# Kernel optimization log

Hardware: AMD Instinct MI355X
Metric: run time of the kernel (lower is better)

## Reference

```python
import jax, jax.numpy as jnp
import numpy as np

B, N, C = 8, 1024, 1024
H = 16
D = C // H  # head_dim = 64
SCALE = D ** -0.5


def setup_inputs() -> dict:
    key = jax.random.key(0)
    k1, k2, k3, k4 = jax.random.split(key, 4)
    x = jax.random.normal(k1, (B, N, C), dtype=jnp.float32)
    qkv_w = jax.random.normal(k2, (3 * C, C), dtype=jnp.float32) * (C ** -0.5)
    proj_w = jax.random.normal(k3, (C, C), dtype=jnp.float32) * (C ** -0.5)
    proj_b = jax.random.normal(k4, (C,), dtype=jnp.float32)
    return {"x": x, "qkv_w": qkv_w, "proj_w": proj_w, "proj_b": proj_b}


def reference(x, qkv_w, proj_w, proj_b):
    # qkv projection: torch Linear weight is [out, in] -> x @ W^T
    qkv = jnp.einsum('bnc,oc->bno', x, qkv_w)            # [B, N, 3C]
    qkv = qkv.reshape(B, N, 3, H, D)
    q = jnp.transpose(qkv[:, :, 0], (0, 2, 1, 3))        # [B, H, N, D]
    k = jnp.transpose(qkv[:, :, 1], (0, 2, 1, 3))
    v = jnp.transpose(qkv[:, :, 2], (0, 2, 1, 3))
    attn = jnp.einsum('bhqd,bhkd->bhqk', q, k) * SCALE   # [B, H, N, N]
    attn = jax.nn.softmax(attn, axis=-1)
    out = jnp.einsum('bhqk,bhkd->bhqd', attn, v)         # [B, H, N, D]
    out = jnp.transpose(out, (0, 2, 1, 3)).reshape(B, N, C)
    out = jnp.einsum('bnc,oc->bno', out, proj_w) + proj_b
    return out
```

## Files before the change

### kernel.cpp

```cpp
#include <hip/hip_runtime.h>
#include <hip/hip_bf16.h>
#include <stdint.h>

#define B_ 8
#define N_ 1024
#define C_ 1024
#define H_ 16

static constexpr float SCALE = 0.125f;
static constexpr float LOG2E = 1.4426950408889634f;
static constexpr float SL    = SCALE * LOG2E;

typedef __attribute__((ext_vector_type(4))) float f32x4;
typedef __attribute__((ext_vector_type(8))) short s16x8;

__device__ __forceinline__ ushort f2bf(float f) {
    union { float f; uint32_t u; } c; c.f = f;
    uint32_t u = c.u;
    return (ushort)((u + 0x7fffu + ((u >> 16) & 1u)) >> 16);
}

__device__ __forceinline__ ushort f2bfc(float f) {
    union { __hip_bfloat16 h; ushort u; } c;
    c.h = __float2bfloat16(f);
    return c.u;
}

__device__ __forceinline__ void gload_lds16(const void* g, void* l) {
    __builtin_amdgcn_global_load_lds(
        (const __attribute__((address_space(1))) void*)g,
        (__attribute__((address_space(3))) void*)l,
        16, 0, 0);
}
__device__ __forceinline__ void gload_lds4(const void* g, void* l) {
    __builtin_amdgcn_global_load_lds(
        (const __attribute__((address_space(1))) void*)g,
        (__attribute__((address_space(3))) void*)l,
        4, 0, 0);
}

__global__ __launch_bounds__(256) void cvt_all(const float* __restrict__ x,
                                               const float* __restrict__ qkv_w,
                                               const float* __restrict__ proj_w,
                                               ushort* __restrict__ xb,
                                               ushort* __restrict__ wqkv,
                                               ushort* __restrict__ wproj) {
    int i = blockIdx.x * 256 + threadIdx.x;
    const float* src;
    ushort* dst;
    float sc = 1.0f;
    if (i < 2097152) {
        src = x; dst = xb;
    } else if (i < 2097152 + 786432) {
        i -= 2097152;
        src = qkv_w; dst = wqkv;
        if (i < 262144) sc = SL;
    } else {
        i -= 2097152 + 786432;
        src = proj_w; dst = wproj;
    }
    float4 v = ((const float4*)src)[i];
    ushort4 o = make_ushort4(f2bf(v.x * sc), f2bf(v.y * sc), f2bf(v.z * sc), f2bf(v.w * sc));
    ((ushort4*)dst)[i] = o;
}

template<int OUT_BF16>
__global__ __launch_bounds__(256) void gemm_bt(const ushort* __restrict__ A,
                                               const ushort* __restrict__ Bw,
                                               void* __restrict__ Cout,
                                               const float* __restrict__ bias,
                                               int M, int Nout, int K) {
    __shared__ ushort Asm[128 * 64];
    __shared__ ushort Bsm[128 * 64];
    const int t = threadIdx.x;
    const int l = t & 63, w = t >> 6;
    const int lq = l & 15, lg = l >> 4;
    const int trow = blockIdx.y * 128, tcol = blockIdx.x * 128;
    const int wrow = (w >> 1) * 64, wcol = (w & 1) * 64;

    f32x4 acc[4][4] = {};

    const int srow0 = t >> 3;
    const int sc8 = (((t & 7) ^ (srow0 & 7)) * 8);
    const size_t abase = (size_t)(trow + srow0) * K + sc8;
    const size_t bbase = (size_t)(tcol + srow0) * K + sc8;

    for (int k0 = 0; k0 < K; k0 += 64) {
#pragma unroll
        for (int i = 0; i < 4; ++i) {
            gload_lds16(A + abase + (size_t)i * 32 * K + k0, &Asm[(i * 256 + w * 64) * 8]);
            gload_lds16(Bw + bbase + (size_t)i * 32 * K + k0, &Bsm[(i * 256 + w * 64) * 8]);
        }
        __syncthreads();
#pragma unroll
        for (int kk = 0; kk < 2; ++kk) {
            s16x8 af[4], bf[4];
#pragma unroll
            for (int m = 0; m < 4; ++m) {
                int row = wrow + m * 16 + lq;
                int ch = (kk * 4 + lg) ^ (row & 7);
                af[m] = *(const s16x8*)&Asm[row * 64 + ch * 8];
            }
#pragma unroll
            for (int n = 0; n < 4; ++n) {
                int row = wcol + n * 16 + lq;
                int ch = (kk * 4 + lg) ^ (row & 7);
                bf[n] = *(const s16x8*)&Bsm[row * 64 + ch * 8];
            }
#pragma unroll
            for (int m = 0; m < 4; ++m)
#pragma unroll
                for (int n = 0; n < 4; ++n)
                    acc[m][n] = __builtin_amdgcn_mfma_f32_16x16x32_bf16(af[m], bf[n], acc[m][n], 0, 0, 0);
        }
        __syncthreads();
    }

#pragma unroll
    for (int m = 0; m < 4; ++m)
#pragma unroll
        for (int n = 0; n < 4; ++n)
#pragma unroll
            for (int r = 0; r < 4; ++r) {
                int row = trow + wrow + m * 16 + lg * 4 + r;
                int col = tcol + wcol + n * 16 + lq;
                if (OUT_BF16) {
                    ((ushort*)Cout)[(size_t)row * Nout + col] = f2bfc(acc[m][n][r]);
                } else {
                    ((float*)Cout)[(size_t)row * Nout + col] = acc[m][n][r] + bias[col];
                }
            }
}

__global__ __launch_bounds__(512, 2) void gemm_bt256(const ushort* __restrict__ A,
                                                     const ushort* __restrict__ Bw,
                                                     ushort* __restrict__ Cout,
                                                     int M, int Nout, int K) {
    __shared__ ushort Asm[2][256 * 64];
    __shared__ ushort Bsm[2][256 * 64];
    const int t = threadIdx.x;
    const int l = t & 63, w = t >> 6;
    const int lq = l & 15, lg = l >> 4;
    const int wm = w >> 2, wn = w & 3;

    int bid = blockIdx.y * gridDim.x + blockIdx.x;
    const int cpx = (gridDim.x * gridDim.y) >> 3;
    bid = (bid & 7) * cpx + (bid >> 3);
    const int bx = bid % gridDim.x, by = bid / gridDim.x;
    const int trow = by * 256, tcol = bx * 256;

    f32x4 acc[8][4] = {};

    const int srow = t >> 3;
    const int scc = ((t & 7) ^ (srow & 7)) * 8;
    const size_t abase = (size_t)(trow + srow) * K + scc;
    const size_t bbase = (size_t)(tcol + srow) * K + scc;

#define STAGE256(buf, k0)                                                      \
    {                                                                          \
        _Pragma("unroll")                                                      \
        for (int j = 0; j < 4; ++j) {                                          \
            gload_lds16(A + abase + (size_t)j * 64 * K + (k0),                 \
                        &Asm[buf][(j * 512 + t) * 8]);                         \
            gload_lds16(Bw + bbase + (size_t)j * 64 * K + (k0),                \
                        &Bsm[buf][(j * 512 + t) * 8]);                         \
        }                                                                      \
    }
#define LOAD_A256(qr)                                                          \
    _Pragma("unroll") for (int m = 0; m < 4; ++m) {                            \
        const int row = wm * 128 + (qr) * 64 + m * 16 + lq;                    \
        _Pragma("unroll") for (int kk = 0; kk < 2; ++kk)                       \
            af[m][kk] = *(const s16x8*)&Asm[cur][row * 64 +                    \
                            (((kk * 4 + lg) ^ (row & 7)) * 8)];                \
    }
#define LOAD_B256(qc)                                                          \
    _Pragma("unroll") for (int n = 0; n < 2; ++n) {                            \
        const int row = wn * 64 + (qc) * 32 + n * 16 + lq;                     \
        _Pragma("unroll") for (int kk = 0; kk < 2; ++kk)                       \
            bf[n][kk] = *(const s16x8*)&Bsm[cur][row * 64 +                    \
                            (((kk * 4 + lg) ^ (row & 7)) * 8)];                \
    }
#define MFMA_Q256(qr, qc)                                                      \
    __builtin_amdgcn_s_setprio(1);                                             \
    _Pragma("unroll") for (int m = 0; m < 4; ++m)                              \
        _Pragma("unroll") for (int n = 0; n < 2; ++n)                          \
            _Pragma("unroll") for (int kk = 0; kk < 2; ++kk)                   \
                acc[(qr) * 4 + m][(qc) * 2 + n] =                              \
                    __builtin_amdgcn_mfma_f32_16x16x32_bf16(                   \
                        af[m][kk], bf[n][kk], acc[(qr) * 4 + m][(qc) * 2 + n], \
                        0, 0, 0);                                              \
    __builtin_amdgcn_s_setprio(0);

    STAGE256(0, 0);
    asm volatile("s_waitcnt vmcnt(0)" ::: "memory");
    __builtin_amdgcn_s_barrier();

    const int NT = K / 64;
    for (int kt = 0; kt < NT; ++kt) {
        const int cur = kt & 1, nxt = cur ^ 1;
        s16x8 af[4][2], bf[2][2];
        LOAD_A256(0); LOAD_B256(0);
        if (kt < NT - 1) STAGE256(nxt, (kt + 1) * 64);
        __builtin_amdgcn_s_barrier();
        MFMA_Q256(0, 0);
        __builtin_amdgcn_s_barrier();
        LOAD_B256(1);
        __builtin_amdgcn_s_barrier();
        MFMA_Q256(0, 1);
        __builtin_amdgcn_s_barrier();
        LOAD_A256(1);
        __builtin_amdgcn_s_barrier();
        MFMA_Q256(1, 1);
        __builtin_amdgcn_s_barrier();
        LOAD_B256(0);
        __builtin_amdgcn_s_barrier();
        MFMA_Q256(1, 0);
        asm volatile("s_waitcnt vmcnt(0)" ::: "memory");
        __builtin_amdgcn_s_barrier();
    }

#pragma unroll
    for (int mt = 0; mt < 8; ++mt)
#pragma unroll
        for (int nt = 0; nt < 4; ++nt)
#pragma unroll
            for (int r = 0; r < 4; ++r) {
                int row = trow + wm * 128 + mt * 16 + lg * 4 + r;
                int col = tcol + wn * 64 + nt * 16 + lq;
                Cout[(size_t)row * Nout + col] = f2bfc(acc[mt][nt][r]);
            }
#undef STAGE256
#undef LOAD_A256
#undef LOAD_B256
#undef MFMA_Q256
}

__global__ __launch_bounds__(512) void attn_fwd(const ushort* __restrict__ qk,
                                                const ushort* __restrict__ vt,
                                                ushort* __restrict__ attn_out) {
    __shared__ ushort Klds[64 * 64];
    __shared__ ushort Vlds[64 * 64];

    const int t = threadIdx.x, l = t & 63, w = t >> 6;
    const int lq = l & 15, lg = l >> 4;

    const int serial = blockIdx.x + 8 * blockIdx.y;
    const int logical = (serial & 7) * 128 + (serial >> 3);
    const int qt = logical & 7;
    const int bh = logical >> 3;
    const int b = bh >> 4, h = bh & 15;

    const int qrow = qt * 128 + w * 16 + lq;
    const size_t qoff = (size_t)(b * N_ + qrow) * 2048 + h * 64;
    const s16x8 qf0 = *(const s16x8*)&qk[qoff + lg * 8];
    const s16x8 qf1 = *(const s16x8*)&qk[qoff + 32 + lg * 8];

    float l_run = 0.f;
    f32x4 o[4] = {};

    const int srow0 = t >> 3;
    const int sc8 = ((t & 7) ^ (srow0 & 7)) * 8;
    const size_t kgbase = (size_t)(b * N_ + srow0) * 2048 + 1024 + h * 64 + sc8;

    const ushort* vptr[4];
#pragma unroll
    for (int j = 0; j < 4; ++j) {
        const int d = 8 * w + 2 * j + (l >> 5);
        const int c = ((l & 31) >> 2) ^ (d & 7);
        const int s = c * 8 + (l & 3) * 2;
        const int key = (s >> 5) * 32 + ((s >> 2) & 1) * 16 + ((s >> 3) & 3) * 4 + (s & 3);
        vptr[j] = vt + (size_t)(h * 64 + d) * (B_ * N_) + b * N_ + key;
    }

    for (int kt = 0; kt < N_ / 64; ++kt) {
        gload_lds16(qk + kgbase + (size_t)kt * 64 * 2048, &Klds[w * 512]);
#pragma unroll
        for (int j = 0; j < 4; ++j)
            gload_lds4(vptr[j] + kt * 64, &Vlds[w * 512 + j * 128]);
        __syncthreads();

        f32x4 s[4];
#pragma unroll
        for (int g = 0; g < 4; ++g) {
            int key = g * 16 + lq;
            const s16x8 kf0 = *(const s16x8*)&Klds[key * 64 + ((lg ^ (key & 7)) * 8)];
            const s16x8 kf1 = *(const s16x8*)&Klds[key * 64 + (((4 + lg) ^ (key & 7)) * 8)];
            f32x4 z = {};
            z    = __builtin_amdgcn_mfma_f32_16x16x32_bf16(kf0, qf0, z, 0, 0, 0);
            s[g] = __builtin_amdgcn_mfma_f32_16x16x32_bf16(kf1, qf1, z, 0, 0, 0);
        }

        float pv[4][4];
        float psum = 0.f;
#pragma unroll
        for (int g = 0; g < 4; ++g) {
            float p0 = __builtin_amdgcn_exp2f(s[g][0]);
            float p1 = __builtin_amdgcn_exp2f(s[g][1]);
            float p2 = __builtin_amdgcn_exp2f(s[g][2]);
            float p3 = __builtin_amdgcn_exp2f(s[g][3]);
            psum += (p0 + p1) + (p2 + p3);
            pv[g][0] = p0; pv[g][1] = p1; pv[g][2] = p2; pv[g][3] = p3;
        }
        l_run += psum;

#pragma unroll
        for (int kb = 0; kb < 2; ++kb) {
            s16x8 pfrag;
#pragma unroll
            for (int i = 0; i < 4; ++i) {
                pfrag[i]     = (short)f2bfc(pv[2 * kb][i]);
                pfrag[4 + i] = (short)f2bfc(pv[2 * kb + 1][i]);
            }
#pragma unroll
            for (int ds = 0; ds < 4; ++ds) {
                const s16x8 vf = *(const s16x8*)
                    &Vlds[(ds * 16 + lq) * 64 + (((kb * 4 + lg) ^ (lq & 7)) * 8)];
                o[ds] = __builtin_amdgcn_mfma_f32_16x16x32_bf16(pfrag, vf, o[ds], 0, 0, 0);
            }
        }
        __syncthreads();
    }

    l_run += __shfl_xor(l_run, 16);
    l_run += __shfl_xor(l_run, 32);

#pragma unroll
    for (int r = 0; r < 4; ++r) {
        float rl = 1.f / __shfl(l_run, lg * 4 + r);
        int orow = qt * 128 + w * 16 + lg * 4 + r;
        size_t base = (size_t)(b * N_ + orow) * C_ + h * 64 + lq;
#pragma unroll
        for (int ds = 0; ds < 4; ++ds)
            attn_out[base + ds * 16] = f2bfc(o[ds][r] * rl);
    }
}

extern "C" void kernel_launch(void* const* d_in, const int* in_sizes, int n_in,
                              void* d_out, int out_size, void* d_ws, size_t ws_size,
                              hipStream_t stream) {
    const float* x      = (const float*)d_in[0];
    const float* qkv_w  = (const float*)d_in[1];
    const float* proj_w = (const float*)d_in[2];
    const float* proj_b = (const float*)d_in[3];
    float* out = (float*)d_out;

    ushort* ws    = (ushort*)d_ws;
    ushort* xb    = ws;
    ushort* wqkv  = xb + (size_t)8192 * 1024;
    ushort* wproj = wqkv + (size_t)3072 * 1024;
    ushort* qkb   = wproj + (size_t)1024 * 1024;
    ushort* vtb   = qkb + (size_t)8192 * 2048;
    ushort* attn  = vtb + (size_t)1024 * 8192;

    cvt_all<<<12288, 256, 0, stream>>>(x, qkv_w, proj_w, xb, wqkv, wproj);

    gemm_bt256<<<dim3(8, 32), 512, 0, stream>>>(xb, wqkv, qkb, 8192, 2048, 1024);
    gemm_bt<1><<<dim3(64, 8), 256, 0, stream>>>(wqkv + (size_t)2048 * 1024, xb, (void*)vtb,
                                                nullptr, 1024, 8192, 1024);

    attn_fwd<<<dim3(8, 128), 512, 0, stream>>>(qkb, vtb, attn);

    gemm_bt<0><<<dim3(8, 64), 256, 0, stream>>>(attn, wproj, (void*)out, proj_b, 8192, 1024, 1024);
}
```

Measured before the change: 154.5 us.

## Process two query tiles per wave in attention to reuse K/V fragments

```diff
diff --git a/kernel.cpp b/kernel.cpp
--- a/kernel.cpp
+++ b/kernel.cpp
@@ -235,28 +235,31 @@
 #undef MFMA_Q256
 }
 
-__global__ __launch_bounds__(512) void attn_fwd(const ushort* __restrict__ qk,
-                                                const ushort* __restrict__ vt,
-                                                ushort* __restrict__ attn_out) {
+__global__ __launch_bounds__(512, 4) void attn_fwd(const ushort* __restrict__ qk,
+                                                   const ushort* __restrict__ vt,
+                                                   ushort* __restrict__ attn_out) {
     __shared__ ushort Klds[64 * 64];
     __shared__ ushort Vlds[64 * 64];
 
     const int t = threadIdx.x, l = t & 63, w = t >> 6;
     const int lq = l & 15, lg = l >> 4;
 
-    const int serial = blockIdx.x + 8 * blockIdx.y;
-    const int logical = (serial & 7) * 128 + (serial >> 3);
-    const int qt = logical & 7;
-    const int bh = logical >> 3;
+    const int serial = blockIdx.x + 4 * blockIdx.y;
+    const int logical = (serial & 7) * 64 + (serial >> 3);
+    const int qt = logical & 3;
+    const int bh = logical >> 2;
     const int b = bh >> 4, h = bh & 15;
 
-    const int qrow = qt * 128 + w * 16 + lq;
-    const size_t qoff = (size_t)(b * N_ + qrow) * 2048 + h * 64;
-    const s16x8 qf0 = *(const s16x8*)&qk[qoff + lg * 8];
-    const s16x8 qf1 = *(const s16x8*)&qk[qoff + 32 + lg * 8];
-
-    float l_run = 0.f;
-    f32x4 o[4] = {};
+    const int qbase = qt * 256 + w * 32 + lq;
+    const size_t qoff0 = (size_t)(b * N_ + qbase) * 2048 + h * 64;
+    const size_t qoff1 = qoff0 + (size_t)16 * 2048;
+    const s16x8 qa0 = *(const s16x8*)&qk[qoff0 + lg * 8];
+    const s16x8 qa1 = *(const s16x8*)&qk[qoff0 + 32 + lg * 8];
+    const s16x8 qb0 = *(const s16x8*)&qk[qoff1 + lg * 8];
+    const s16x8 qb1 = *(const s16x8*)&qk[qoff1 + 32 + lg * 8];
+
+    float lr0 = 0.f, lr1 = 0.f;
+    f32x4 o0[4] = {}, o1[4] = {};
 
     const int srow0 = t >> 3;
     const int sc8 = ((t & 7) ^ (srow0 & 7)) * 8;
@@ -279,59 +282,59 @@
             gload_lds4(vptr[j] + kt * 64, &Vlds[w * 512 + j * 128]);
         __syncthreads();
 
-        f32x4 s[4];
+        f32x4 s0[4], s1[4];
 #pragma unroll
         for (int g = 0; g < 4; ++g) {
             int key = g * 16 + lq;
             const s16x8 kf0 = *(const s16x8*)&Klds[key * 64 + ((lg ^ (key & 7)) * 8)];
             const s16x8 kf1 = *(const s16x8*)&Klds[key * 64 + (((4 + lg) ^ (key & 7)) * 8)];
-            f32x4 z = {};
-            z    = __builtin_amdgcn_mfma_f32_16x16x32_bf16(kf0, qf0, z, 0, 0, 0);
-            s[g] = __builtin_amdgcn_mfma_f32_16x16x32_bf16(kf1, qf1, z, 0, 0, 0);
-        }
-
-        float pv[4][4];
-        float psum = 0.f;
-#pragma unroll
-        for (int g = 0; g < 4; ++g) {
-            float p0 = __builtin_amdgcn_exp2f(s[g][0]);
-            float p1 = __builtin_amdgcn_exp2f(s[g][1]);
-            float p2 = __builtin_amdgcn_exp2f(s[g][2]);
-            float p3 = __builtin_amdgcn_exp2f(s[g][3]);
-            psum += (p0 + p1) + (p2 + p3);
-            pv[g][0] = p0; pv[g][1] = p1; pv[g][2] = p2; pv[g][3] = p3;
-        }
-        l_run += psum;
+            f32x4 z0 = {}, z1 = {};
+            z0    = __builtin_amdgcn_mfma_f32_16x16x32_bf16(kf0, qa0, z0, 0, 0, 0);
+            s0[g] = __builtin_amdgcn_mfma_f32_16x16x32_bf16(kf1, qa1, z0, 0, 0, 0);
+            z1    = __builtin_amdgcn_mfma_f32_16x16x32_bf16(kf0, qb0, z1, 0, 0, 0);
+            s1[g] = __builtin_amdgcn_mfma_f32_16x16x32_bf16(kf1, qb1, z1, 0, 0, 0);
+        }
 
 #pragma unroll
         for (int kb = 0; kb < 2; ++kb) {
-            s16x8 pfrag;
+            s16x8 pf0, pf1;
 #pragma unroll
             for (int i = 0; i < 4; ++i) {
-                pfrag[i]     = (short)f2bfc(pv[2 * kb][i]);
-                pfrag[4 + i] = (short)f2bfc(pv[2 * kb + 1][i]);
+                float a0 = __builtin_amdgcn_exp2f(s0[2 * kb][i]);
+                float a1 = __builtin_amdgcn_exp2f(s0[2 * kb + 1][i]);
+                float b0 = __builtin_amdgcn_exp2f(s1[2 * kb][i]);
+                float b1 = __builtin_amdgcn_exp2f(s1[2 * kb + 1][i]);
+                lr0 += a0 + a1;
+                lr1 += b0 + b1;
+                pf0[i] = (short)f2bfc(a0); pf0[4 + i] = (short)f2bfc(a1);
+                pf1[i] = (short)f2bfc(b0); pf1[4 + i] = (short)f2bfc(b1);
             }
 #pragma unroll
             for (int ds = 0; ds < 4; ++ds) {
                 const s16x8 vf = *(const s16x8*)
                     &Vlds[(ds * 16 + lq) * 64 + (((kb * 4 + lg) ^ (lq & 7)) * 8)];
-                o[ds] = __builtin_amdgcn_mfma_f32_16x16x32_bf16(pfrag, vf, o[ds], 0, 0, 0);
+                o0[ds] = __builtin_amdgcn_mfma_f32_16x16x32_bf16(pf0, vf, o0[ds], 0, 0, 0);
+                o1[ds] = __builtin_amdgcn_mfma_f32_16x16x32_bf16(pf1, vf, o1[ds], 0, 0, 0);
             }
         }
         __syncthreads();
     }
 
-    l_run += __shfl_xor(l_run, 16);
-    l_run += __shfl_xor(l_run, 32);
+    lr0 += __shfl_xor(lr0, 16); lr0 += __shfl_xor(lr0, 32);
+    lr1 += __shfl_xor(lr1, 16); lr1 += __shfl_xor(lr1, 32);
 
 #pragma unroll
     for (int r = 0; r < 4; ++r) {
-        float rl = 1.f / __shfl(l_run, lg * 4 + r);
-        int orow = qt * 128 + w * 16 + lg * 4 + r;
-        size_t base = (size_t)(b * N_ + orow) * C_ + h * 64 + lq;
-#pragma unroll
-        for (int ds = 0; ds < 4; ++ds)
-            attn_out[base + ds * 16] = f2bfc(o[ds][r] * rl);
+        float rl0 = 1.f / __shfl(lr0, lg * 4 + r);
+        float rl1 = 1.f / __shfl(lr1, lg * 4 + r);
+        int orow = qt * 256 + w * 32 + lg * 4 + r;
+        size_t base0 = (size_t)(b * N_ + orow) * C_ + h * 64 + lq;
+        size_t base1 = base0 + (size_t)16 * C_;
+#pragma unroll
+        for (int ds = 0; ds < 4; ++ds) {
+            attn_out[base0 + ds * 16] = f2bfc(o0[ds][r] * rl0);
+            attn_out[base1 + ds * 16] = f2bfc(o1[ds][r] * rl1);
+        }
     }
 }
 
@@ -358,7 +361,7 @@
     gemm_bt<1><<<dim3(64, 8), 256, 0, stream>>>(wqkv + (size_t)2048 * 1024, xb, (void*)vtb,
                                                 nullptr, 1024, 8192, 1024);
 
-    attn_fwd<<<dim3(8, 128), 512, 0, stream>>>(qkb, vtb, attn);
+    attn_fwd<<<dim3(4, 128), 512, 0, stream>>>(qkb, vtb, attn);
 
     gemm_bt<0><<<dim3(8, 64), 256, 0, stream>>>(attn, wproj, (void*)out, proj_b, 8192, 1024, 1024);
 }
```

After: 145.1 us. -6.0%, faster.
